# Kernel tuning notes

Measured on AMD Instinct MI355X. Metric: run time of the kernel, lower is better.

Reference implementation:

```python
import jax, jax.numpy as jnp
import numpy as np

P1 = np.array([[700.0, 0.0, 128.0, 102400.0], [0.0, 700.0, 128.0, 102400.0], [0.0, 0.0, 1.0, 800.0]])
P2 = np.array([[-128.0, 0.0, 700.0, 102400.0], [-128.0, 700.0, 0.0, 102400.0], [-1.0, 0.0, 0.0, 800.0]])


def _calculate_fundamental_matrix(P_src, P_dst):
    # camera center of source view = right null vector of P_src
    _, _, Vt = np.linalg.svd(P_src)
    C = Vt[-1]
    C = C / C[-1]
    e2 = P_dst @ C  # epipole in destination view
    ex = np.array([[0.0, -e2[2], e2[1]], [e2[2], 0.0, -e2[0]], [-e2[1], e2[0], 0.0]])
    F = ex @ P_dst @ np.linalg.pinv(P_src)
    return F / np.linalg.norm(F)  # scale-invariant for epipolar lines


def setup_inputs() -> dict:
    key = jax.random.key(0)
    x = jax.random.normal(key, (2, 8, 256, 256), dtype=jnp.float32)
    F21 = jnp.asarray(_calculate_fundamental_matrix(P1, P2), dtype=jnp.float32)
    return {"input": x, "F": F21}


def _translate(img, F):
    # For each output pixel p=(u,v,1) (destination view), the epipolar line in the
    # source image is l = F^T p (since x_dst^T F x_src = 0). The kernel integrates
    # (nearest-neighbor line rasterization, dominant-axis sweep) the source image
    # along that line -> output (B,C,H,W).
    B, C, Hs, Ws = img.shape
    Ho, Wo = Hs, Ws
    uu, vv = jnp.meshgrid(jnp.arange(Wo, dtype=img.dtype), jnp.arange(Ho, dtype=img.dtype))  # (Ho,Wo)
    p = jnp.stack([uu, vv, jnp.ones_like(uu)])            # (3,Ho,Wo) homogeneous pixels
    l = jnp.einsum('ji,jhw->ihw', F, p)                    # F^T p -> line coeffs (3,Ho,Wo)
    a, b, c = l[0], l[1], l[2]
    eps = jnp.asarray(1e-8, img.dtype)
    b_safe = jnp.where(jnp.abs(b) < eps, eps, b)
    a_safe = jnp.where(jnp.abs(a) < eps, eps, a)
    zeros = jnp.zeros((B, C, Ho, Wo), img.dtype)

    def col_step(acc, x):
        xf = x.astype(img.dtype)
        y = -(a * xf + c) / b_safe                         # (Ho,Wo)
        yi = jnp.round(y).astype(jnp.int32)
        valid = (yi >= 0) & (yi < Hs)
        samp = img[:, :, jnp.clip(yi, 0, Hs - 1), x]       # gather -> (B,C,Ho,Wo)
        return acc + jnp.where(valid, samp, jnp.zeros((), img.dtype)), None

    def row_step(acc, y):
        yf = y.astype(img.dtype)
        x = -(b * yf + c) / a_safe                         # (Ho,Wo)
        xi = jnp.round(x).astype(jnp.int32)
        valid = (xi >= 0) & (xi < Ws)
        samp = img[:, :, y, jnp.clip(xi, 0, Ws - 1)]       # gather -> (B,C,Ho,Wo)
        return acc + jnp.where(valid, samp, jnp.zeros((), img.dtype)), None

    sum_col, _ = jax.lax.scan(col_step, zeros, jnp.arange(Ws))
    sum_row, _ = jax.lax.scan(row_step, zeros, jnp.arange(Hs))
    use_col = jnp.abs(b) >= jnp.abs(a)                     # dominant-axis selection per pixel
    return jnp.where(use_col, sum_col, sum_row)


def reference(input, F):
    assert input.ndim == 4
    return _translate(input, F)
```

## Files before the change

kernel.cpp:

```cpp
#include <hip/hip_runtime.h>
#include <hip/hip_fp16.h>

#define HS 256
#define WSZ 256
#define NPIX (HS * WSZ)
#define NCH 16
#define NELEM (NPIX * NCH)

typedef float f4 __attribute__((ext_vector_type(4)));

__global__ __launch_bounds__(256) void transpose_f16(const float* __restrict__ x,
                                                     __half* __restrict__ T) {
    __shared__ float lds[16][257];
    int tid  = threadIdx.x;
    int base = blockIdx.x * 256;
#pragma unroll
    for (int ch = 0; ch < 16; ++ch)
        lds[ch][tid] = x[ch * NPIX + base + tid];
    if (blockIdx.x == 0 && tid < 128)
        ((unsigned int*)(T + NELEM))[tid] = 0u;
    __syncthreads();
    uint2* T2 = (uint2*)T;
#pragma unroll
    for (int it = 0; it < 4; ++it) {
        int idx = it * 256 + tid;
        int p   = idx >> 2;
        int q   = idx & 3;
        __half2 a = __floats2half2_rn(lds[q * 4 + 0][p], lds[q * 4 + 1][p]);
        __half2 b = __floats2half2_rn(lds[q * 4 + 2][p], lds[q * 4 + 3][p]);
        uint2 o;
        o.x = __builtin_bit_cast(unsigned int, a);
        o.y = __builtin_bit_cast(unsigned int, b);
        T2[base * 4 + idx] = o;
    }
}

struct LineGeom {
    float p, q, c;
    bool  col;
};

__device__ __forceinline__ LineGeom make_geom(const float* __restrict__ F, int pix) {
#pragma clang fp contract(off)
    int w = pix & (WSZ - 1);
    int h = pix >> 8;
    float u = (float)w, v = (float)h;
    float a = __builtin_fmaf(F[3], v, F[0] * u) + F[6];
    float b = __builtin_fmaf(F[4], v, F[1] * u) + F[7];
    float c = __builtin_fmaf(F[5], v, F[2] * u) + F[8];
    const float eps = 1e-8f;
    float bs = (fabsf(b) < eps) ? eps : b;
    float as = (fabsf(a) < eps) ? eps : a;
    LineGeom g;
    g.col = (fabsf(b) >= fabsf(a));
    g.p   = g.col ? a : b;
    g.q   = g.col ? bs : as;
    g.c   = c;
    return g;
}

__device__ __forceinline__ int chainY(const LineGeom& g, int s) {
#pragma clang fp contract(off)
    float t  = __builtin_fmaf(g.p, (float)s, g.c);
    float y  = (-t) / g.q;
    return (int)__builtin_rintf(y);
}

__device__ __forceinline__ __half2 bch2(unsigned int v) {
    return __builtin_bit_cast(__half2, v);
}

#define QUAD_BCAST(dst, src, ctrl)                                              \
    dst = __builtin_amdgcn_mov_dpp(src, ctrl, 0xf, 0xf, false)

__global__ __launch_bounds__(256) void epi_gather_f16(const uint4* __restrict__ Tq,
                                                      const float* __restrict__ x,
                                                      const float* __restrict__ F,
                                                      float* __restrict__ out) {
    int tid = blockIdx.x * 256 + threadIdx.x;
    int r   = tid & 15;
    int k   = r >> 1;
    int h   = r & 1;
    int pix = tid >> 4;

    LineGeom g = make_geom(F, pix);
    f4 a0 = {0.f, 0.f, 0.f, 0.f};
    f4 a1 = {0.f, 0.f, 0.f, 0.f};

    if (g.col) {
        const int PADB = NPIX * 2;
        int  padr = PADB + r;
        int  rb   = r;
        bool hb   = (h != 0);
        int  sb   = (h << 5) + k;

#pragma unroll
        for (int b = 0; b < 4; ++b) {
            int yown[4], yswp[4];
#pragma unroll
            for (int i = 0; i < 4; ++i) yown[i] = chainY(g, sb + 64 * b + 8 * i);
#pragma unroll
            for (int i = 0; i < 4; ++i) QUAD_BCAST(yswp[i], yown[i], 0xB1);

            int adr[8];
#pragma unroll
            for (int i = 0; i < 4; ++i) {
                int ylo = hb ? yswp[i] : yown[i];
                int yhi = hb ? yown[i] : yswp[i];
                int alo = (int)((unsigned)ylo << 9) + rb;
                int ahi = (int)((unsigned)yhi << 9) + rb;
                adr[i]     = ((unsigned)ylo < 256u) ? alo : (padr - 16 * i);
                adr[i + 4] = ((unsigned)yhi < 256u) ? ahi : (padr - 16 * (i + 4));
            }
            uint4 v0 = Tq[adr[0] +   0];
            uint4 v1 = Tq[adr[1] +  16];
            uint4 v2 = Tq[adr[2] +  32];
            uint4 v3 = Tq[adr[3] +  48];
            uint4 v4 = Tq[adr[4] +  64];
            uint4 v5 = Tq[adr[5] +  80];
            uint4 v6 = Tq[adr[6] +  96];
            uint4 v7 = Tq[adr[7] + 112];

            __half2 zz = __floats2half2_rn(0.f, 0.f);
            __half2 s0 = zz, s1 = zz, s2 = zz, s3 = zz;
#define ACC(V)                                                                  \
            s0 = __hadd2(s0, bch2((V).x));                                      \
            s1 = __hadd2(s1, bch2((V).y));                                      \
            s2 = __hadd2(s2, bch2((V).z));                                      \
            s3 = __hadd2(s3, bch2((V).w));
            ACC(v0) ACC(v1) ACC(v2) ACC(v3) ACC(v4) ACC(v5) ACC(v6) ACC(v7)
#undef ACC
            float2 f;
            f = __half22float2(s0); a0.x += f.x; a0.y += f.y;
            f = __half22float2(s1); a0.z += f.x; a0.w += f.y;
            f = __half22float2(s2); a1.x += f.x; a1.y += f.y;
            f = __half22float2(s3); a1.z += f.x; a1.w += f.y;

            rb += 128;
        }
    } else {
        int ch0 = h * 8;
        for (int m = 0; m < 32; ++m) {
            int s  = 8 * m + k;
            int xi = chainY(g, s);
            if ((unsigned)xi < 256u) {
                int addr = s * WSZ + xi;
                a0.x += x[(ch0 + 0) * NPIX + addr];
                a0.y += x[(ch0 + 1) * NPIX + addr];
                a0.z += x[(ch0 + 2) * NPIX + addr];
                a0.w += x[(ch0 + 3) * NPIX + addr];
                a1.x += x[(ch0 + 4) * NPIX + addr];
                a1.y += x[(ch0 + 5) * NPIX + addr];
                a1.z += x[(ch0 + 6) * NPIX + addr];
                a1.w += x[(ch0 + 7) * NPIX + addr];
            }
        }
    }

#pragma unroll
    for (int d = 2; d <= 8; d <<= 1) {
        a0.x += __shfl_xor(a0.x, d, 64);
        a0.y += __shfl_xor(a0.y, d, 64);
        a0.z += __shfl_xor(a0.z, d, 64);
        a0.w += __shfl_xor(a0.w, d, 64);
        a1.x += __shfl_xor(a1.x, d, 64);
        a1.y += __shfl_xor(a1.y, d, 64);
        a1.z += __shfl_xor(a1.z, d, 64);
        a1.w += __shfl_xor(a1.w, d, 64);
    }

    if ((r & 14) == 0) {
        int ch0 = h * 8;
        out[(ch0 + 0) * NPIX + pix] = a0.x;
        out[(ch0 + 1) * NPIX + pix] = a0.y;
        out[(ch0 + 2) * NPIX + pix] = a0.z;
        out[(ch0 + 3) * NPIX + pix] = a0.w;
        out[(ch0 + 4) * NPIX + pix] = a1.x;
        out[(ch0 + 5) * NPIX + pix] = a1.y;
        out[(ch0 + 6) * NPIX + pix] = a1.z;
        out[(ch0 + 7) * NPIX + pix] = a1.w;
    }
}

__global__ __launch_bounds__(256) void epi_gather_direct(const float* __restrict__ x,
                                                         const float* __restrict__ F,
                                                         float* __restrict__ out) {
    int tid  = blockIdx.x * 256 + threadIdx.x;
    int quad = tid & 3;
    int pix  = tid >> 2;

    LineGeom g = make_geom(F, pix);

    float4 acc = make_float4(0.f, 0.f, 0.f, 0.f);
    int base = quad * 4;

#pragma unroll 2
    for (int s = 0; s < 256; ++s) {
        int  yi    = chainY(g, s);
        bool valid = ((unsigned)yi < 256u);
        int  tcl   = valid ? yi : 0;
        int  addr  = g.col ? (tcl * WSZ + s) : (s * WSZ + tcl);
        if (valid) {
            acc.x += x[(base + 0) * NPIX + addr];
            acc.y += x[(base + 1) * NPIX + addr];
            acc.z += x[(base + 2) * NPIX + addr];
            acc.w += x[(base + 3) * NPIX + addr];
        }
    }

    out[(base + 0) * NPIX + pix] = acc.x;
    out[(base + 1) * NPIX + pix] = acc.y;
    out[(base + 2) * NPIX + pix] = acc.z;
    out[(base + 3) * NPIX + pix] = acc.w;
}

extern "C" void kernel_launch(void* const* d_in, const int* in_sizes, int n_in,
                              void* d_out, int out_size, void* d_ws, size_t ws_size,
                              hipStream_t stream) {
    const float* x   = (const float*)d_in[0];
    const float* F   = (const float*)d_in[1];
    float*       out = (float*)d_out;

    const size_t need = (size_t)NELEM * sizeof(__half) + 512;
    if (ws_size >= need) {
        __half* T = (__half*)d_ws;
        transpose_f16<<<NPIX / 256, 256, 0, stream>>>(x, T);
        epi_gather_f16<<<(NPIX * 16) / 256, 256, 0, stream>>>((const uint4*)T, x, F, out);
    } else {
        epi_gather_direct<<<(NPIX * 4) / 256, 256, 0, stream>>>(x, F, out);
    }
}
```

Measured before the change: 80.61 us.

## Use reciprocal-based line stepping, longer fp16 accumulation, and DPP row-rotate reduction

Replaces the per-sample float division in the column path with a Newton-refined reciprocal multiply, falling back to exact division only near rounding ties. It also accumulates two sample batches in fp16 before converting to fp32, and swaps the shfl_xor cross-lane reduction for DPP row_ror adds. These target division latency, conversion overhead and LDS-based shuffle cost. In exchange they risk rounding mismatches near .5 boundaries and lower fp16 accumulation precision, and they rely on the DPP rotate and the xor reduction giving the same sums for the lanes that write output.

```diff
diff --git a/kernel.cpp b/kernel.cpp
--- a/kernel.cpp
+++ b/kernel.cpp
@@ -66,8 +66,38 @@
     return (int)__builtin_rintf(y);
 }
 
+__device__ __forceinline__ int chainY_fast(const LineGeom& g, float rq, int s) {
+#pragma clang fp contract(off)
+    float num = __builtin_fmaf(-g.p, (float)s, -g.c);
+    float y0  = num * rq;
+    float e   = __builtin_fmaf(-g.q, y0, num);
+    float y1  = __builtin_fmaf(e, rq, y0);
+    float fr  = y1 - floorf(y1);
+    if (__builtin_expect(fabsf(fr - 0.5f) < 2e-4f, 0))
+        y1 = num / g.q;
+    return (int)__builtin_rintf(y1);
+}
+
 __device__ __forceinline__ __half2 bch2(unsigned int v) {
     return __builtin_bit_cast(__half2, v);
+}
+
+template <int CTRL>
+__device__ __forceinline__ float dpp_ror_add(float v) {
+    int t = __builtin_amdgcn_mov_dpp(__builtin_bit_cast(int, v), CTRL, 0xf, 0xf, true);
+    return v + __builtin_bit_cast(float, t);
+}
+
+template <int CTRL>
+__device__ __forceinline__ void ror_add8(f4& a0, f4& a1) {
+    a0.x = dpp_ror_add<CTRL>(a0.x);
+    a0.y = dpp_ror_add<CTRL>(a0.y);
+    a0.z = dpp_ror_add<CTRL>(a0.z);
+    a0.w = dpp_ror_add<CTRL>(a0.w);
+    a1.x = dpp_ror_add<CTRL>(a1.x);
+    a1.y = dpp_ror_add<CTRL>(a1.y);
+    a1.z = dpp_ror_add<CTRL>(a1.z);
+    a1.w = dpp_ror_add<CTRL>(a1.w);
 }
 
 #define QUAD_BCAST(dst, src, ctrl)                                              \
@@ -88,6 +118,9 @@
     f4 a1 = {0.f, 0.f, 0.f, 0.f};
 
     if (g.col) {
+        float r0 = __builtin_amdgcn_rcpf(g.q);
+        float rq = __builtin_fmaf(__builtin_fmaf(-g.q, r0, 1.0f), r0, r0);
+
         const int PADB = NPIX * 2;
         int  padr = PADB + r;
         int  rb   = r;
@@ -95,48 +128,53 @@
         int  sb   = (h << 5) + k;
 
 #pragma unroll
-        for (int b = 0; b < 4; ++b) {
-            int yown[4], yswp[4];
-#pragma unroll
-            for (int i = 0; i < 4; ++i) yown[i] = chainY(g, sb + 64 * b + 8 * i);
-#pragma unroll
-            for (int i = 0; i < 4; ++i) QUAD_BCAST(yswp[i], yown[i], 0xB1);
-
-            int adr[8];
-#pragma unroll
-            for (int i = 0; i < 4; ++i) {
-                int ylo = hb ? yswp[i] : yown[i];
-                int yhi = hb ? yown[i] : yswp[i];
-                int alo = (int)((unsigned)ylo << 9) + rb;
-                int ahi = (int)((unsigned)yhi << 9) + rb;
-                adr[i]     = ((unsigned)ylo < 256u) ? alo : (padr - 16 * i);
-                adr[i + 4] = ((unsigned)yhi < 256u) ? ahi : (padr - 16 * (i + 4));
-            }
-            uint4 v0 = Tq[adr[0] +   0];
-            uint4 v1 = Tq[adr[1] +  16];
-            uint4 v2 = Tq[adr[2] +  32];
-            uint4 v3 = Tq[adr[3] +  48];
-            uint4 v4 = Tq[adr[4] +  64];
-            uint4 v5 = Tq[adr[5] +  80];
-            uint4 v6 = Tq[adr[6] +  96];
-            uint4 v7 = Tq[adr[7] + 112];
-
+        for (int bb = 0; bb < 2; ++bb) {
             __half2 zz = __floats2half2_rn(0.f, 0.f);
             __half2 s0 = zz, s1 = zz, s2 = zz, s3 = zz;
+
+#pragma unroll
+            for (int b2 = 0; b2 < 2; ++b2) {
+                int b = 2 * bb + b2;
+                int yown[4], yswp[4];
+#pragma unroll
+                for (int i = 0; i < 4; ++i)
+                    yown[i] = chainY_fast(g, rq, sb + 64 * b + 8 * i);
+#pragma unroll
+                for (int i = 0; i < 4; ++i) QUAD_BCAST(yswp[i], yown[i], 0xB1);
+
+                int adr[8];
+#pragma unroll
+                for (int i = 0; i < 4; ++i) {
+                    int ylo = hb ? yswp[i] : yown[i];
+                    int yhi = hb ? yown[i] : yswp[i];
+                    int alo = (int)((unsigned)ylo << 9) + rb;
+                    int ahi = (int)((unsigned)yhi << 9) + rb;
+                    adr[i]     = ((unsigned)ylo < 256u) ? alo : (padr - 16 * i);
+                    adr[i + 4] = ((unsigned)yhi < 256u) ? ahi : (padr - 16 * (i + 4));
+                }
+                uint4 v0 = Tq[adr[0] +   0];
+                uint4 v1 = Tq[adr[1] +  16];
+                uint4 v2 = Tq[adr[2] +  32];
+                uint4 v3 = Tq[adr[3] +  48];
+                uint4 v4 = Tq[adr[4] +  64];
+                uint4 v5 = Tq[adr[5] +  80];
+                uint4 v6 = Tq[adr[6] +  96];
+                uint4 v7 = Tq[adr[7] + 112];
+
 #define ACC(V)                                                                  \
-            s0 = __hadd2(s0, bch2((V).x));                                      \
-            s1 = __hadd2(s1, bch2((V).y));                                      \
-            s2 = __hadd2(s2, bch2((V).z));                                      \
-            s3 = __hadd2(s3, bch2((V).w));
-            ACC(v0) ACC(v1) ACC(v2) ACC(v3) ACC(v4) ACC(v5) ACC(v6) ACC(v7)
+                s0 = __hadd2(s0, bch2((V).x));                                  \
+                s1 = __hadd2(s1, bch2((V).y));                                  \
+                s2 = __hadd2(s2, bch2((V).z));                                  \
+                s3 = __hadd2(s3, bch2((V).w));
+                ACC(v0) ACC(v1) ACC(v2) ACC(v3) ACC(v4) ACC(v5) ACC(v6) ACC(v7)
 #undef ACC
+                rb += 128;
+            }
             float2 f;
             f = __half22float2(s0); a0.x += f.x; a0.y += f.y;
             f = __half22float2(s1); a0.z += f.x; a0.w += f.y;
             f = __half22float2(s2); a1.x += f.x; a1.y += f.y;
             f = __half22float2(s3); a1.z += f.x; a1.w += f.y;
-
-            rb += 128;
         }
     } else {
         int ch0 = h * 8;
@@ -157,17 +195,9 @@
         }
     }
 
-#pragma unroll
-    for (int d = 2; d <= 8; d <<= 1) {
-        a0.x += __shfl_xor(a0.x, d, 64);
-        a0.y += __shfl_xor(a0.y, d, 64);
-        a0.z += __shfl_xor(a0.z, d, 64);
-        a0.w += __shfl_xor(a0.w, d, 64);
-        a1.x += __shfl_xor(a1.x, d, 64);
-        a1.y += __shfl_xor(a1.y, d, 64);
-        a1.z += __shfl_xor(a1.z, d, 64);
-        a1.w += __shfl_xor(a1.w, d, 64);
-    }
+    ror_add8<0x128>(a0, a1);
+    ror_add8<0x124>(a0, a1);
+    ror_add8<0x122>(a0, a1);
 
     if ((r & 14) == 0) {
         int ch0 = h * 8;
```

Result: no change. 80.36 us (median of 2 runs) (-0.3%).
